# Kernel tuning notes

Measured on AMD Instinct MI355X. Metric: run time of the kernel, lower is better.

## Reference

```python
import jax, jax.numpy as jnp
import numpy as np

B, S, H = 8, 1024, 16
DV = 1024      # video_input_dim
LAT = 1024     # latent_dim
DQ = LAT // H  # query_dim = 64
DH = 64        # head_dim


def setup_inputs() -> dict:
    key = jax.random.key(0)
    ks = jax.random.split(key, 12)
    sc = lambda fan_in: 1.0 / np.sqrt(fan_in)
    return {
        "input": jax.random.normal(ks[0], (B, S, DV), jnp.float32),
        "latent": jax.random.normal(ks[1], (B, S, LAT), jnp.float32),
        "attention_mask": jax.random.randint(ks[2], (B * H, S, S), 0, 2, jnp.int32),
        "Wq": jax.random.normal(ks[3], (LAT, H * DQ), jnp.float32) * sc(LAT),
        "bq": jnp.zeros((H * DQ,), jnp.float32),
        "Wk": jax.random.normal(ks[4], (DV, H * DQ), jnp.float32) * sc(DV),
        "bk": jnp.zeros((H * DQ,), jnp.float32),
        "Wv": jax.random.normal(ks[5], (DV, H * DH), jnp.float32) * sc(DV),
        "bv": jnp.zeros((H * DH,), jnp.float32),
        "Wo": jax.random.normal(ks[6], (H * DH, LAT), jnp.float32) * sc(H * DH),
        "bo": jnp.zeros((LAT,), jnp.float32),
    }


def reference(input, latent, attention_mask, Wq, bq, Wk, bk, Wv, bv, Wo, bo):
    b, s, _ = input.shape
    # projections -> [b, h, s, d]
    q = (latent @ Wq + bq).reshape(b, s, H, DQ).transpose(0, 2, 1, 3)
    k = (input @ Wk + bk).reshape(b, s, H, DQ).transpose(0, 2, 1, 3)
    v = (input @ Wv + bv).reshape(b, s, H, DH).transpose(0, 2, 1, 3)
    # [b, h, s, s] score matrix (materialized, as in the original bmm)
    scores = jnp.einsum("bhqd,bhkd->bhqk", q, k) / jnp.sqrt(jnp.float32(DQ))
    mask = attention_mask.reshape(b, H, s, s)
    scores = jnp.where(mask == 0, -jnp.inf, scores)
    weights = jax.nn.softmax(scores, axis=-1)
    out = jnp.einsum("bhqk,bhkd->bhqd", weights, v)  # [b, h, s, dh]
    out = out.transpose(0, 2, 1, 3).reshape(b, s, H * DH)
    return out @ Wo + bo
```

## Files before the change

### kernel.cpp

```cpp
#include <hip/hip_runtime.h>
#include <hip/hip_bf16.h>
#include <stdint.h>

typedef __bf16 bf16;
typedef __bf16 bf16x8 __attribute__((ext_vector_type(8)));
typedef float f32x4 __attribute__((ext_vector_type(4)));
typedef unsigned short u16;
typedef unsigned short u16x4 __attribute__((ext_vector_type(4)));


__device__ __forceinline__ void gld16(const bf16* g, bf16* l) {
    __builtin_amdgcn_global_load_lds(
        (const __attribute__((address_space(1))) void*)g,
        (__attribute__((address_space(3))) void*)l, 16, 0, 0);
}

__global__ __launch_bounds__(256) void prep(
        const float* __restrict__ input, const float* __restrict__ latent,
        bf16* __restrict__ Xb, bf16* __restrict__ Lb,
        const float* __restrict__ w0, const float* __restrict__ w1,
        const float* __restrict__ w2, const float* __restrict__ w3,
        bf16* __restrict__ t0, bf16* __restrict__ t1,
        bf16* __restrict__ t2, bf16* __restrict__ t3) {
    __shared__ float tile[32][33];
    const int bid = blockIdx.x;
    const int tid = threadIdx.x;
    if (bid < 4096) {
        const float* src = (bid >> 11) ? latent : input;
        bf16* dst = (bid >> 11) ? Lb : Xb;
        const int nchunk = (8 * 1024 * 1024) / 4;
        for (int c = (bid & 2047) * 256 + tid; c < nchunk; c += 2048 * 256) {
            float4 v = *(const float4*)&src[(size_t)c * 4];
            u16x4 o;
            o[0] = __builtin_bit_cast(u16, (bf16)v.x);
            o[1] = __builtin_bit_cast(u16, (bf16)v.y);
            o[2] = __builtin_bit_cast(u16, (bf16)v.z);
            o[3] = __builtin_bit_cast(u16, (bf16)v.w);
            *(u16x4*)&dst[(size_t)c * 4] = o;
        }
    } else {
        const int tb = bid - 4096;
        const float* src; bf16* dst;
        switch (tb >> 10) {
            case 0:  src = w0; dst = t0; break;
            case 1:  src = w1; dst = t1; break;
            case 2:  src = w2; dst = t2; break;
            default: src = w3; dst = t3; break;
        }
        const int r  = tb & 1023;
        const int bx = r & 31, by = r >> 5;
        const int tx = tid & 31, ty = tid >> 5;
        const int x = bx * 32 + tx;
        const int y = by * 32 + ty;
        #pragma unroll
        for (int j = 0; j < 32; j += 8)
            tile[ty + j][tx] = src[(size_t)(y + j) * 1024 + x];
        __syncthreads();
        const int x2 = by * 32 + tx;
        const int y2 = bx * 32 + ty;
        #pragma unroll
        for (int j = 0; j < 32; j += 8)
            dst[(size_t)(y2 + j) * 1024 + x2] = (bf16)tile[tx][ty + j];
    }
}

__device__ __forceinline__ void gemm_core(const bf16* __restrict__ X,
                                          const bf16* __restrict__ Wt,
                                          const float* __restrict__ bias,
                                          void* __restrict__ outv, int mode,
                                          int m0, int n0, bf16* Al, bf16* Bl) {
    const int tid  = threadIdx.x;
    const int lane = tid & 63;
    const int w    = tid >> 6;
    const int wm   = (w & 1) * 64;
    const int wn   = (w >> 1) * 64;
    const int l15  = lane & 15;
    const int quad = lane >> 4;
    const int sw   = (l15 >> 1) & 3;

    f32x4 acc[4][4] = {};

    for (int kt = 0; kt < 1024; kt += 32) {
        __syncthreads();
        #pragma unroll
        for (int t = 0; t < 2; t++) {
            int c = (w * 2 + t) * 64 + lane;
            int row = c >> 2;
            int e   = (c & 3) ^ ((c >> 3) & 3);
            gld16(&X [(size_t)(m0 + row) * 1024 + kt + e * 8], &Al[(w * 2 + t) * 512]);
            gld16(&Wt[(size_t)(n0 + row) * 1024 + kt + e * 8], &Bl[(w * 2 + t) * 512]);
        }
        __syncthreads();
        bf16x8 a[4], b[4];
        #pragma unroll
        for (int i = 0; i < 4; i++)
            a[i] = *(const bf16x8*)&Al[(wm + i * 16 + l15) * 32 + (quad ^ sw) * 8];
        #pragma unroll
        for (int j = 0; j < 4; j++)
            b[j] = *(const bf16x8*)&Bl[(wn + j * 16 + l15) * 32 + (quad ^ sw) * 8];
        #pragma unroll
        for (int i = 0; i < 4; i++)
            #pragma unroll
            for (int j = 0; j < 4; j++)
                acc[i][j] = __builtin_amdgcn_mfma_f32_16x16x32_bf16(a[i], b[j], acc[i][j], 0, 0, 0);
    }

    float bv[4];
    #pragma unroll
    for (int j = 0; j < 4; j++) bv[j] = bias[n0 + wn + j * 16 + l15];

    #pragma unroll
    for (int i = 0; i < 4; i++) {
        int mbase = m0 + wm + i * 16 + quad * 4;
        #pragma unroll
        for (int j = 0; j < 4; j++) {
            int n = n0 + wn + j * 16 + l15;
            if (mode == 2) {
                bf16* out = (bf16*)outv;
                int b = mbase >> 10, s = mbase & 1023;
                int h = n >> 6, d = n & 63;
                u16x4 pack;
                #pragma unroll
                for (int r = 0; r < 4; r++) {
                    bf16 v = (bf16)(acc[i][j][r] + bv[j]);
                    pack[r] = __builtin_bit_cast(u16, v);
                }
                *(u16x4*)&out[(((size_t)(b * 16 + h)) * 64 + d) * 1024 + s] = pack;
            } else if (mode == 1) {
                bf16* out = (bf16*)outv;
                #pragma unroll
                for (int r = 0; r < 4; r++) {
                    int m = mbase + r;
                    int b = m >> 10, s = m & 1023;
                    int h = n >> 6, d = n & 63;
                    out[(((size_t)(b * 16 + h)) * 1024 + s) * 64 + d] =
                        (bf16)(acc[i][j][r] + bv[j]);
                }
            } else {
                float* out = (float*)outv;
                #pragma unroll
                for (int r = 0; r < 4; r++)
                    out[(size_t)(mbase + r) * 1024 + n] = acc[i][j][r] + bv[j];
            }
        }
    }
}

__global__ __launch_bounds__(256, 3) void gemm_qkv(
        const bf16* __restrict__ Lb, const bf16* __restrict__ Xb,
        const bf16* __restrict__ Wqt, const bf16* __restrict__ Wkt,
        const bf16* __restrict__ Wvt,
        const float* __restrict__ bq, const float* __restrict__ bk,
        const float* __restrict__ bv,
        bf16* __restrict__ Qh, bf16* __restrict__ Kh, bf16* __restrict__ Vt) {
    __shared__ bf16 Al[128 * 32];
    __shared__ bf16 Bl[128 * 32];
    const bf16* X; const bf16* Wt; const float* bias; void* out; int mode;
    switch (blockIdx.z) {
        case 0:  X = Lb; Wt = Wqt; bias = bq; out = Qh; mode = 1; break;
        case 1:  X = Xb; Wt = Wkt; bias = bk; out = Kh; mode = 1; break;
        default: X = Xb; Wt = Wvt; bias = bv; out = Vt; mode = 2; break;
    }
    gemm_core(X, Wt, bias, out, mode, blockIdx.x * 128, blockIdx.y * 128, Al, Bl);
}

__global__ __launch_bounds__(256, 3) void gemm_o(
        const bf16* __restrict__ Ob, const bf16* __restrict__ Wot,
        const float* __restrict__ bo, float* __restrict__ out) {
    __shared__ bf16 Al[128 * 32];
    __shared__ bf16 Bl[128 * 32];
    gemm_core(Ob, Wot, bo, out, 0, blockIdx.x * 128, blockIdx.y * 128, Al, Bl);
}

__global__ __launch_bounds__(256, 3) void attn(const bf16* __restrict__ Q,
                                               const bf16* __restrict__ K,
                                               const bf16* __restrict__ Vt,
                                               const int*  __restrict__ mask,
                                               bf16* __restrict__ O) {
    __shared__ bf16 Kl[2][4096];
    __shared__ bf16 Vl[2][4096];
    __shared__ bf16 Pl[4][32 * 68];

    const int tid  = threadIdx.x;
    const int lane = tid & 63;
    const int w    = tid >> 6;
    const int l15  = lane & 15;
    const int quad = lane >> 4;

    const int blk = blockIdx.x;
    const int bh  = (blk & 7) * 16 + (blk >> 6);
    const int q0  = ((blk >> 3) & 7) * 128;
    const int qrow0 = q0 + w * 32;

    const bf16* Kbh = K  + (size_t)bh * 65536;
    const bf16* Vbh = Vt + (size_t)bh * 65536;
    const int* mbase = mask + ((size_t)bh * 1024 + qrow0 + quad * 4) * 1024;

    bf16x8 qa[2][2];
    #pragma unroll
    for (int rb = 0; rb < 2; rb++) {
        const bf16* Qb = Q + ((size_t)bh * 1024 + qrow0 + rb * 16 + l15) * 64;
        qa[rb][0] = *(const bf16x8*)&Qb[quad * 8];
        qa[rb][1] = *(const bf16x8*)&Qb[32 + quad * 8];
    }

    const int c0 = (w * 2 + 0) * 64 + lane;
    const int c1 = (w * 2 + 1) * 64 + lane;
    const int swz = l15 & 7;

    #define STAGE_KV(kk, buf)                                                          \
        {                                                                              \
            int r0 = c0 >> 3, e0 = (c0 & 7) ^ (r0 & 7);                                \
            int r1 = c1 >> 3, e1 = (c1 & 7) ^ (r1 & 7);                                \
            gld16(&Kbh[(size_t)((kk) + r0) * 64 + e0 * 8], &Kl[buf][(w * 2 + 0) * 512]); \
            gld16(&Kbh[(size_t)((kk) + r1) * 64 + e1 * 8], &Kl[buf][(w * 2 + 1) * 512]); \
            gld16(&Vbh[(size_t)r0 * 1024 + (kk) + e0 * 8], &Vl[buf][(w * 2 + 0) * 512]); \
            gld16(&Vbh[(size_t)r1 * 1024 + (kk) + e1 * 8], &Vl[buf][(w * 2 + 1) * 512]); \
        }

    STAGE_KV(0, 0);
    int mn[2][4][4];
    #pragma unroll
    for (int rb = 0; rb < 2; rb++)
        #pragma unroll
        for (int r = 0; r < 4; r++)
            #pragma unroll
            for (int t = 0; t < 4; t++)
                mn[rb][r][t] = mbase[(size_t)(rb * 16 + r) * 1024 + t * 16 + l15];

    f32x4 o[2][4] = {};
    float lsum[2][4] = {};
    bf16* Pw = Pl[w];

    for (int it = 0; it < 16; it++) {
        __syncthreads();
        const int cur = it & 1, nxt = cur ^ 1;
        const int kn = ((it + 1) & 15) * 64;

        int nib[2][4];
        #pragma unroll
        for (int rb = 0; rb < 2; rb++)
            #pragma unroll
            for (int r = 0; r < 4; r++)
                nib[rb][r] = (mn[rb][r][0] != 0) | ((mn[rb][r][1] != 0) << 1) |
                             ((mn[rb][r][2] != 0) << 2) | ((mn[rb][r][3] != 0) << 3);

        STAGE_KV(kn, nxt);
        #pragma unroll
        for (int rb = 0; rb < 2; rb++)
            #pragma unroll
            for (int r = 0; r < 4; r++)
                #pragma unroll
                for (int t = 0; t < 4; t++)
                    mn[rb][r][t] = mbase[(size_t)(rb * 16 + r) * 1024 + kn + t * 16 + l15];

        f32x4 s[2][4];
        #pragma unroll
        for (int t = 0; t < 4; t++) {
            bf16x8 kb0 = *(const bf16x8*)&Kl[cur][(t * 16 + l15) * 64 + ((0 + quad) ^ swz) * 8];
            bf16x8 kb1 = *(const bf16x8*)&Kl[cur][(t * 16 + l15) * 64 + ((4 + quad) ^ swz) * 8];
            #pragma unroll
            for (int rb = 0; rb < 2; rb++) {
                f32x4 z = {};
                z = __builtin_amdgcn_mfma_f32_16x16x32_bf16(qa[rb][0], kb0, z, 0, 0, 0);
                z = __builtin_amdgcn_mfma_f32_16x16x32_bf16(qa[rb][1], kb1, z, 0, 0, 0);
                s[rb][t] = z;
            }
        }

        #pragma unroll
        for (int rb = 0; rb < 2; rb++)
            #pragma unroll
            for (int t = 0; t < 4; t++)
                #pragma unroll
                for (int r = 0; r < 4; r++) {
                    float p = __expf(fmaf(s[rb][t][r], 0.125f, -12.0f));
                    p = ((nib[rb][r] >> t) & 1) ? p : 0.0f;
                    lsum[rb][r] += p;
                    Pw[(rb * 16 + quad * 4 + r) * 68 + t * 16 + l15] = (bf16)p;
                }

        bf16x8 pa[2][2];
        #pragma unroll
        for (int rb = 0; rb < 2; rb++) {
            pa[rb][0] = *(const bf16x8*)&Pw[(rb * 16 + l15) * 68 + quad * 8];
            pa[rb][1] = *(const bf16x8*)&Pw[(rb * 16 + l15) * 68 + 32 + quad * 8];
        }
        #pragma unroll
        for (int nt = 0; nt < 4; nt++) {
            bf16x8 vb0 = *(const bf16x8*)&Vl[cur][(nt * 16 + l15) * 64 + ((0 + quad) ^ swz) * 8];
            bf16x8 vb1 = *(const bf16x8*)&Vl[cur][(nt * 16 + l15) * 64 + ((4 + quad) ^ swz) * 8];
            #pragma unroll
            for (int rb = 0; rb < 2; rb++) {
                o[rb][nt] = __builtin_amdgcn_mfma_f32_16x16x32_bf16(pa[rb][0], vb0, o[rb][nt], 0, 0, 0);
                o[rb][nt] = __builtin_amdgcn_mfma_f32_16x16x32_bf16(pa[rb][1], vb1, o[rb][nt], 0, 0, 0);
            }
        }
    }
    #undef STAGE_KV

    const int b = bh >> 4, h = bh & 15;
    #pragma unroll
    for (int rb = 0; rb < 2; rb++)
        #pragma unroll
        for (int r = 0; r < 4; r++) {
            float l = lsum[rb][r];
            #pragma unroll
            for (int off = 1; off < 16; off <<= 1)
                l += __shfl_xor(l, off, 64);
            float inv = 1.0f / l;
            int srow = qrow0 + rb * 16 + quad * 4 + r;
            bf16* orow = O + ((size_t)(b * 1024 + srow)) * 1024 + h * 64;
            #pragma unroll
            for (int nt = 0; nt < 4; nt++)
                orow[nt * 16 + l15] = (bf16)(o[rb][nt][r] * inv);
        }
}

extern "C" void kernel_launch(void* const* d_in, const int* in_sizes, int n_in,
                              void* d_out, int out_size, void* d_ws, size_t ws_size,
                              hipStream_t stream) {
    const float* input  = (const float*)d_in[0];
    const float* latent = (const float*)d_in[1];
    const int*   mask   = (const int*)d_in[2];
    const float* Wq = (const float*)d_in[3];
    const float* bq = (const float*)d_in[4];
    const float* Wk = (const float*)d_in[5];
    const float* bk = (const float*)d_in[6];
    const float* Wv = (const float*)d_in[7];
    const float* bv = (const float*)d_in[8];
    const float* Wo = (const float*)d_in[9];
    const float* bo = (const float*)d_in[10];
    float* out = (float*)d_out;

    char* ws = (char*)d_ws;
    bf16* Xb  = (bf16*)(ws);
    bf16* Lb  = (bf16*)(ws + (16u << 20));
    bf16* Qh  = (bf16*)(ws + (32u << 20));
    bf16* Kh  = (bf16*)(ws + (48u << 20));
    bf16* Vt  = (bf16*)(ws + (64u << 20));
    bf16* Ob  = (bf16*)(ws + (80u << 20));
    bf16* Wqt = (bf16*)(ws + (96u << 20));
    bf16* Wkt = (bf16*)(ws + (98u << 20));
    bf16* Wvt = (bf16*)(ws + (100u << 20));
    bf16* Wot = (bf16*)(ws + (102u << 20));

    prep<<<dim3(8192, 1, 1), 256, 0, stream>>>(
        input, latent, Xb, Lb, Wq, Wk, Wv, Wo, Wqt, Wkt, Wvt, Wot);

    gemm_qkv<<<dim3(64, 8, 3), 256, 0, stream>>>(
        Lb, Xb, Wqt, Wkt, Wvt, bq, bk, bv, Qh, Kh, Vt);

    attn<<<dim3(1024, 1, 1), 256, 0, stream>>>(Qh, Kh, Vt, mask, Ob);

    gemm_o<<<dim3(64, 8, 1), 256, 0, stream>>>(Ob, Wot, bo, out);
}
```

Before: 935.3 us.

## Pack attention mask into bitmasks inside QKV GEMM launch, read bits in attention

Adds a fourth role to the fused QKV GEMM kernel in which some blocks read the int32 attention mask and compress it with ballots into 64-bit words per row and key tile. The attention kernel then loads one u64 per row per tile instead of 16 int32 values. Packing runs concurrently with the GEMM blocks, so the heavy mask read can overlap compute. The GEMM mode becomes a template parameter and launch bounds change (attn 2 waves/SIMD hint). The mask is still read in full once, and the packing adds a write-then-read through a small workspace buffer.

```diff
diff --git a/kernel.cpp b/kernel.cpp
--- a/kernel.cpp
+++ b/kernel.cpp
@@ -7,6 +7,7 @@
 typedef float f32x4 __attribute__((ext_vector_type(4)));
 typedef unsigned short u16;
 typedef unsigned short u16x4 __attribute__((ext_vector_type(4)));
+typedef unsigned long long u64;
 
 
 __device__ __forceinline__ void gld16(const bf16* g, bf16* l) {
@@ -64,10 +65,11 @@
     }
 }
 
+template<int MODE>
 __device__ __forceinline__ void gemm_core(const bf16* __restrict__ X,
                                           const bf16* __restrict__ Wt,
                                           const float* __restrict__ bias,
-                                          void* __restrict__ outv, int mode,
+                                          void* __restrict__ outv,
                                           int m0, int n0, bf16* Al, bf16* Bl) {
     const int tid  = threadIdx.x;
     const int lane = tid & 63;
@@ -115,7 +117,7 @@
         #pragma unroll
         for (int j = 0; j < 4; j++) {
             int n = n0 + wn + j * 16 + l15;
-            if (mode == 2) {
+            if (MODE == 2) {
                 bf16* out = (bf16*)outv;
                 int b = mbase >> 10, s = mbase & 1023;
                 int h = n >> 6, d = n & 63;
@@ -126,7 +128,7 @@
                     pack[r] = __builtin_bit_cast(u16, v);
                 }
                 *(u16x4*)&out[(((size_t)(b * 16 + h)) * 64 + d) * 1024 + s] = pack;
-            } else if (mode == 1) {
+            } else if (MODE == 1) {
                 bf16* out = (bf16*)outv;
                 #pragma unroll
                 for (int r = 0; r < 4; r++) {
@@ -146,36 +148,55 @@
     }
 }
 
-__global__ __launch_bounds__(256, 3) void gemm_qkv(
+__global__ __launch_bounds__(256) void qkv_pack(
         const bf16* __restrict__ Lb, const bf16* __restrict__ Xb,
         const bf16* __restrict__ Wqt, const bf16* __restrict__ Wkt,
         const bf16* __restrict__ Wvt,
         const float* __restrict__ bq, const float* __restrict__ bk,
         const float* __restrict__ bv,
-        bf16* __restrict__ Qh, bf16* __restrict__ Kh, bf16* __restrict__ Vt) {
+        bf16* __restrict__ Qh, bf16* __restrict__ Kh, bf16* __restrict__ Vt,
+        const int* __restrict__ mask, u64* __restrict__ cmp) {
     __shared__ bf16 Al[128 * 32];
     __shared__ bf16 Bl[128 * 32];
-    const bf16* X; const bf16* Wt; const float* bias; void* out; int mode;
-    switch (blockIdx.z) {
-        case 0:  X = Lb; Wt = Wqt; bias = bq; out = Qh; mode = 1; break;
-        case 1:  X = Xb; Wt = Wkt; bias = bk; out = Kh; mode = 1; break;
-        default: X = Xb; Wt = Wvt; bias = bv; out = Vt; mode = 2; break;
-    }
-    gemm_core(X, Wt, bias, out, mode, blockIdx.x * 128, blockIdx.y * 128, Al, Bl);
-}
-
-__global__ __launch_bounds__(256, 3) void gemm_o(
+    const int bid  = blockIdx.x;
+    const int role = (bid >> 3) & 3;
+    const int sub  = ((bid >> 5) << 3) | (bid & 7);
+
+    if (role == 3) {
+        const int w = threadIdx.x >> 6, lane = threadIdx.x & 63;
+        const int pair = sub * 4 + w;
+        const int bh = pair >> 4, kt = pair & 15;
+        const int perm = 16 * (lane & 3) + (lane >> 2);
+        const int* mrow = mask + ((size_t)bh << 20) + kt * 64 + perm;
+        u64* crow = cmp + ((size_t)(bh * 16 + kt) << 10);
+        #pragma unroll 4
+        for (int row = 0; row < 1024; row++) {
+            int m = mrow[(size_t)row << 10];
+            u64 bal = __ballot(m != 0);
+            if (lane == 0) crow[row] = bal;
+        }
+        return;
+    }
+
+    const int m0 = (sub & 63) * 128;
+    const int n0 = (sub >> 6) * 128;
+    if (role == 0)      gemm_core<1>(Lb, Wqt, bq, Qh, m0, n0, Al, Bl);
+    else if (role == 1) gemm_core<1>(Xb, Wkt, bk, Kh, m0, n0, Al, Bl);
+    else                gemm_core<2>(Xb, Wvt, bv, Vt, m0, n0, Al, Bl);
+}
+
+__global__ __launch_bounds__(256) void gemm_o(
         const bf16* __restrict__ Ob, const bf16* __restrict__ Wot,
         const float* __restrict__ bo, float* __restrict__ out) {
     __shared__ bf16 Al[128 * 32];
     __shared__ bf16 Bl[128 * 32];
-    gemm_core(Ob, Wot, bo, out, 0, blockIdx.x * 128, blockIdx.y * 128, Al, Bl);
-}
-
-__global__ __launch_bounds__(256, 3) void attn(const bf16* __restrict__ Q,
+    gemm_core<0>(Ob, Wot, bo, out, blockIdx.x * 128, blockIdx.y * 128, Al, Bl);
+}
+
+__global__ __launch_bounds__(256, 2) void attn(const bf16* __restrict__ Q,
                                                const bf16* __restrict__ K,
                                                const bf16* __restrict__ Vt,
-                                               const int*  __restrict__ mask,
+                                               const u64*  __restrict__ cmp,
                                                bf16* __restrict__ O) {
     __shared__ bf16 Kl[2][4096];
     __shared__ bf16 Vl[2][4096];
@@ -194,7 +215,7 @@
 
     const bf16* Kbh = K  + (size_t)bh * 65536;
     const bf16* Vbh = Vt + (size_t)bh * 65536;
-    const int* mbase = mask + ((size_t)bh * 1024 + qrow0 + quad * 4) * 1024;
+    const u64*  cw  = cmp + ((size_t)bh << 14);
 
     bf16x8 qa[2][2];
     #pragma unroll
@@ -207,6 +228,7 @@
     const int c0 = (w * 2 + 0) * 64 + lane;
     const int c1 = (w * 2 + 1) * 64 + lane;
     const int swz = l15 & 7;
+    const int sh4 = l15 * 4;
 
     #define STAGE_KV(kk, buf)                                                          \
         {                                                                              \
@@ -219,14 +241,12 @@
         }
 
     STAGE_KV(0, 0);
-    int mn[2][4][4];
+    u64 mw[2][4];
     #pragma unroll
     for (int rb = 0; rb < 2; rb++)
         #pragma unroll
         for (int r = 0; r < 4; r++)
-            #pragma unroll
-            for (int t = 0; t < 4; t++)
-                mn[rb][r][t] = mbase[(size_t)(rb * 16 + r) * 1024 + t * 16 + l15];
+            mw[rb][r] = cw[qrow0 + rb * 16 + quad * 4 + r];
 
     f32x4 o[2][4] = {};
     float lsum[2][4] = {};
@@ -242,17 +262,17 @@
         for (int rb = 0; rb < 2; rb++)
             #pragma unroll
             for (int r = 0; r < 4; r++)
-                nib[rb][r] = (mn[rb][r][0] != 0) | ((mn[rb][r][1] != 0) << 1) |
-                             ((mn[rb][r][2] != 0) << 2) | ((mn[rb][r][3] != 0) << 3);
+                nib[rb][r] = (int)(mw[rb][r] >> sh4) & 15;
 
         STAGE_KV(kn, nxt);
-        #pragma unroll
-        for (int rb = 0; rb < 2; rb++)
-            #pragma unroll
-            for (int r = 0; r < 4; r++)
-                #pragma unroll
-                for (int t = 0; t < 4; t++)
-                    mn[rb][r][t] = mbase[(size_t)(rb * 16 + r) * 1024 + kn + t * 16 + l15];
+        {
+            const u64* cn = cw + (((it + 1) & 15) << 10);
+            #pragma unroll
+            for (int rb = 0; rb < 2; rb++)
+                #pragma unroll
+                for (int r = 0; r < 4; r++)
+                    mw[rb][r] = cn[qrow0 + rb * 16 + quad * 4 + r];
+        }
 
         f32x4 s[2][4];
         #pragma unroll
@@ -344,14 +364,15 @@
     bf16* Wkt = (bf16*)(ws + (98u << 20));
     bf16* Wvt = (bf16*)(ws + (100u << 20));
     bf16* Wot = (bf16*)(ws + (102u << 20));
+    u64*  cmp = (u64*) (ws + (104u << 20));
 
     prep<<<dim3(8192, 1, 1), 256, 0, stream>>>(
         input, latent, Xb, Lb, Wq, Wk, Wv, Wo, Wqt, Wkt, Wvt, Wot);
 
-    gemm_qkv<<<dim3(64, 8, 3), 256, 0, stream>>>(
-        Lb, Xb, Wqt, Wkt, Wvt, bq, bk, bv, Qh, Kh, Vt);
-
-    attn<<<dim3(1024, 1, 1), 256, 0, stream>>>(Qh, Kh, Vt, mask, Ob);
+    qkv_pack<<<dim3(2048, 1, 1), 256, 0, stream>>>(
+        Lb, Xb, Wqt, Wkt, Wvt, bq, bk, bv, Qh, Kh, Vt, mask, cmp);
+
+    attn<<<dim3(1024, 1, 1), 256, 0, stream>>>(Qh, Kh, Vt, cmp, Ob);
 
     gemm_o<<<dim3(64, 8, 1), 256, 0, stream>>>(Ob, Wot, bo, out);
 }
```

Result: slower. 2.185 ms (+133.6%).

## Triple-buffer attention K/V staging with explicit vmcnt waits and MFMA priority

Applied to the files above, without the earlier changes.

The attention kernel moves from double to triple buffering of K/V tiles in LDS. It prefetches two tiles ahead and replaces __syncthreads with a partial s_waitcnt vmcnt plus a raw barrier, and raises wave priority around the MFMA sections. The GEMM core is templated on output mode so each instantiation drops the runtime branch, and the occupancy hints in launch bounds are relaxed (attn now requests 2 blocks per CU). The aim is to hide global-load latency behind compute. It costs more LDS and lower occupancy, and the hand-tuned vmcnt count relies on a specific count of outstanding loads per iteration.

```diff
diff --git a/kernel.cpp b/kernel.cpp
--- a/kernel.cpp
+++ b/kernel.cpp
@@ -64,10 +64,11 @@
     }
 }
 
+template<int MODE>
 __device__ __forceinline__ void gemm_core(const bf16* __restrict__ X,
                                           const bf16* __restrict__ Wt,
                                           const float* __restrict__ bias,
-                                          void* __restrict__ outv, int mode,
+                                          void* __restrict__ outv,
                                           int m0, int n0, bf16* Al, bf16* Bl) {
     const int tid  = threadIdx.x;
     const int lane = tid & 63;
@@ -115,7 +116,7 @@
         #pragma unroll
         for (int j = 0; j < 4; j++) {
             int n = n0 + wn + j * 16 + l15;
-            if (mode == 2) {
+            if (MODE == 2) {
                 bf16* out = (bf16*)outv;
                 int b = mbase >> 10, s = mbase & 1023;
                 int h = n >> 6, d = n & 63;
@@ -126,7 +127,7 @@
                     pack[r] = __builtin_bit_cast(u16, v);
                 }
                 *(u16x4*)&out[(((size_t)(b * 16 + h)) * 64 + d) * 1024 + s] = pack;
-            } else if (mode == 1) {
+            } else if (MODE == 1) {
                 bf16* out = (bf16*)outv;
                 #pragma unroll
                 for (int r = 0; r < 4; r++) {
@@ -146,7 +147,7 @@
     }
 }
 
-__global__ __launch_bounds__(256, 3) void gemm_qkv(
+__global__ __launch_bounds__(256) void gemm_qkv(
         const bf16* __restrict__ Lb, const bf16* __restrict__ Xb,
         const bf16* __restrict__ Wqt, const bf16* __restrict__ Wkt,
         const bf16* __restrict__ Wvt,
@@ -155,30 +156,27 @@
         bf16* __restrict__ Qh, bf16* __restrict__ Kh, bf16* __restrict__ Vt) {
     __shared__ bf16 Al[128 * 32];
     __shared__ bf16 Bl[128 * 32];
-    const bf16* X; const bf16* Wt; const float* bias; void* out; int mode;
-    switch (blockIdx.z) {
-        case 0:  X = Lb; Wt = Wqt; bias = bq; out = Qh; mode = 1; break;
-        case 1:  X = Xb; Wt = Wkt; bias = bk; out = Kh; mode = 1; break;
-        default: X = Xb; Wt = Wvt; bias = bv; out = Vt; mode = 2; break;
-    }
-    gemm_core(X, Wt, bias, out, mode, blockIdx.x * 128, blockIdx.y * 128, Al, Bl);
-}
-
-__global__ __launch_bounds__(256, 3) void gemm_o(
+    const int m0 = blockIdx.x * 128, n0 = blockIdx.y * 128;
+    if (blockIdx.z == 0)      gemm_core<1>(Lb, Wqt, bq, Qh, m0, n0, Al, Bl);
+    else if (blockIdx.z == 1) gemm_core<1>(Xb, Wkt, bk, Kh, m0, n0, Al, Bl);
+    else                      gemm_core<2>(Xb, Wvt, bv, Vt, m0, n0, Al, Bl);
+}
+
+__global__ __launch_bounds__(256) void gemm_o(
         const bf16* __restrict__ Ob, const bf16* __restrict__ Wot,
         const float* __restrict__ bo, float* __restrict__ out) {
     __shared__ bf16 Al[128 * 32];
     __shared__ bf16 Bl[128 * 32];
-    gemm_core(Ob, Wot, bo, out, 0, blockIdx.x * 128, blockIdx.y * 128, Al, Bl);
-}
-
-__global__ __launch_bounds__(256, 3) void attn(const bf16* __restrict__ Q,
+    gemm_core<0>(Ob, Wot, bo, out, blockIdx.x * 128, blockIdx.y * 128, Al, Bl);
+}
+
+__global__ __launch_bounds__(256, 2) void attn(const bf16* __restrict__ Q,
                                                const bf16* __restrict__ K,
                                                const bf16* __restrict__ Vt,
                                                const int*  __restrict__ mask,
                                                bf16* __restrict__ O) {
-    __shared__ bf16 Kl[2][4096];
-    __shared__ bf16 Vl[2][4096];
+    __shared__ bf16 Kl[3][4096];
+    __shared__ bf16 Vl[3][4096];
     __shared__ bf16 Pl[4][32 * 68];
 
     const int tid  = threadIdx.x;
@@ -195,14 +193,6 @@
     const bf16* Kbh = K  + (size_t)bh * 65536;
     const bf16* Vbh = Vt + (size_t)bh * 65536;
     const int* mbase = mask + ((size_t)bh * 1024 + qrow0 + quad * 4) * 1024;
-
-    bf16x8 qa[2][2];
-    #pragma unroll
-    for (int rb = 0; rb < 2; rb++) {
-        const bf16* Qb = Q + ((size_t)bh * 1024 + qrow0 + rb * 16 + l15) * 64;
-        qa[rb][0] = *(const bf16x8*)&Qb[quad * 8];
-        qa[rb][1] = *(const bf16x8*)&Qb[32 + quad * 8];
-    }
 
     const int c0 = (w * 2 + 0) * 64 + lane;
     const int c1 = (w * 2 + 1) * 64 + lane;
@@ -218,6 +208,13 @@
             gld16(&Vbh[(size_t)r1 * 1024 + (kk) + e1 * 8], &Vl[buf][(w * 2 + 1) * 512]); \
         }
 
+    bf16x8 qa[2][2];
+    #pragma unroll
+    for (int rb = 0; rb < 2; rb++) {
+        const bf16* Qb = Q + ((size_t)bh * 1024 + qrow0 + rb * 16 + l15) * 64;
+        qa[rb][0] = *(const bf16x8*)&Qb[quad * 8];
+        qa[rb][1] = *(const bf16x8*)&Qb[32 + quad * 8];
+    }
     STAGE_KV(0, 0);
     int mn[2][4][4];
     #pragma unroll
@@ -227,15 +224,17 @@
             #pragma unroll
             for (int t = 0; t < 4; t++)
                 mn[rb][r][t] = mbase[(size_t)(rb * 16 + r) * 1024 + t * 16 + l15];
+    STAGE_KV(64, 1);
 
     f32x4 o[2][4] = {};
     float lsum[2][4] = {};
     bf16* Pw = Pl[w];
+    int cur = 0, stg = 2;
 
     for (int it = 0; it < 16; it++) {
-        __syncthreads();
-        const int cur = it & 1, nxt = cur ^ 1;
-        const int kn = ((it + 1) & 15) * 64;
+        asm volatile("s_waitcnt vmcnt(8)" ::: "memory");
+        __builtin_amdgcn_s_barrier();
+        __builtin_amdgcn_sched_barrier(0);
 
         int nib[2][4];
         #pragma unroll
@@ -245,20 +244,27 @@
                 nib[rb][r] = (mn[rb][r][0] != 0) | ((mn[rb][r][1] != 0) << 1) |
                              ((mn[rb][r][2] != 0) << 2) | ((mn[rb][r][3] != 0) << 3);
 
-        STAGE_KV(kn, nxt);
-        #pragma unroll
-        for (int rb = 0; rb < 2; rb++)
-            #pragma unroll
-            for (int r = 0; r < 4; r++)
-                #pragma unroll
-                for (int t = 0; t < 4; t++)
-                    mn[rb][r][t] = mbase[(size_t)(rb * 16 + r) * 1024 + kn + t * 16 + l15];
+        {
+            const int kn1 = ((it + 1) & 15) * 64;
+            #pragma unroll
+            for (int rb = 0; rb < 2; rb++)
+                #pragma unroll
+                for (int r = 0; r < 4; r++)
+                    #pragma unroll
+                    for (int t = 0; t < 4; t++)
+                        mn[rb][r][t] = mbase[(size_t)(rb * 16 + r) * 1024 + kn1 + t * 16 + l15];
+        }
+        STAGE_KV(((it + 2) & 15) * 64, stg);
+
+        const bf16* Kc = Kl[cur];
+        const bf16* Vc = Vl[cur];
 
         f32x4 s[2][4];
+        __builtin_amdgcn_s_setprio(1);
         #pragma unroll
         for (int t = 0; t < 4; t++) {
-            bf16x8 kb0 = *(const bf16x8*)&Kl[cur][(t * 16 + l15) * 64 + ((0 + quad) ^ swz) * 8];
-            bf16x8 kb1 = *(const bf16x8*)&Kl[cur][(t * 16 + l15) * 64 + ((4 + quad) ^ swz) * 8];
+            bf16x8 kb0 = *(const bf16x8*)&Kc[(t * 16 + l15) * 64 + ((0 + quad) ^ swz) * 8];
+            bf16x8 kb1 = *(const bf16x8*)&Kc[(t * 16 + l15) * 64 + ((4 + quad) ^ swz) * 8];
             #pragma unroll
             for (int rb = 0; rb < 2; rb++) {
                 f32x4 z = {};
@@ -267,6 +273,7 @@
                 s[rb][t] = z;
             }
         }
+        __builtin_amdgcn_s_setprio(0);
 
         #pragma unroll
         for (int rb = 0; rb < 2; rb++)
@@ -286,16 +293,21 @@
             pa[rb][0] = *(const bf16x8*)&Pw[(rb * 16 + l15) * 68 + quad * 8];
             pa[rb][1] = *(const bf16x8*)&Pw[(rb * 16 + l15) * 68 + 32 + quad * 8];
         }
+        __builtin_amdgcn_s_setprio(1);
         #pragma unroll
         for (int nt = 0; nt < 4; nt++) {
-            bf16x8 vb0 = *(const bf16x8*)&Vl[cur][(nt * 16 + l15) * 64 + ((0 + quad) ^ swz) * 8];
-            bf16x8 vb1 = *(const bf16x8*)&Vl[cur][(nt * 16 + l15) * 64 + ((4 + quad) ^ swz) * 8];
+            bf16x8 vb0 = *(const bf16x8*)&Vc[(nt * 16 + l15) * 64 + ((0 + quad) ^ swz) * 8];
+            bf16x8 vb1 = *(const bf16x8*)&Vc[(nt * 16 + l15) * 64 + ((4 + quad) ^ swz) * 8];
             #pragma unroll
             for (int rb = 0; rb < 2; rb++) {
                 o[rb][nt] = __builtin_amdgcn_mfma_f32_16x16x32_bf16(pa[rb][0], vb0, o[rb][nt], 0, 0, 0);
                 o[rb][nt] = __builtin_amdgcn_mfma_f32_16x16x32_bf16(pa[rb][1], vb1, o[rb][nt], 0, 0, 0);
             }
         }
+        __builtin_amdgcn_s_setprio(0);
+
+        cur = (cur == 2) ? 0 : cur + 1;
+        stg = (stg == 2) ? 0 : stg + 1;
     }
     #undef STAGE_KV
 
```

After: 895.3 us. 4.3% less time.
